# Performance work log

Hardware: AMD Instinct MI355X
Metric: run time of the kernel (lower is better)

Reference implementation:

```python
import jax, jax.numpy as jnp
import numpy as np

SCALE_FACTOR = 1.0
VIS_MAX = 1024


def setup_inputs() -> dict:
    key = jax.random.key(0)
    kq, kk, kv = jax.random.split(key, 3)
    B, C, H, W = 4, 256, 64, 64
    Q = jax.random.normal(kq, (B, C, H, W), dtype=jnp.float32)
    K = jax.random.normal(kk, (B, C, H, W), dtype=jnp.float32)
    V = jax.random.normal(kv, (B, C, H, W), dtype=jnp.float32)
    return {"Q": Q, "K": K, "V": V}


def reference(Q, K, V):
    # Q,K: [B,C,H,W] -> flatten spatial dims to HW
    B, C, H, W = Q.shape
    HW = H * W
    Q_flat = Q.reshape(B, C, HW).transpose(0, 2, 1)  # [B, HW, C]
    K_flat = K.reshape(B, C, HW)                      # [B, C, HW]
    # Full scaled score matrix [B, HW, HW]; argmax over keys reproduces the
    # chunked running-max/argmax (strict '>' update keeps first max, matching
    # jnp.argmax tie-breaking).
    S = jnp.einsum('bqc,bck->bqk', Q_flat, K_flat) * SCALE_FACTOR
    H_idx = jnp.argmax(S, axis=2).astype(jnp.int64)   # [B, HW]
    vis = min(VIS_MAX, HW)
    S_vis = S[:, :vis, :vis]                          # [B, vis, vis]
    return S_vis, H_idx
```

## Files before the change

### kernel.cpp

```cpp
#include <hip/hip_runtime.h>
#include <stdint.h>

#define B_   4
#define C_   256
#define HW_  4096
#define VIS_ 1024
#define KE_  768

using half8   = __attribute__((ext_vector_type(8))) _Float16;
using floatx4 = __attribute__((ext_vector_type(4))) float;

__device__ __forceinline__ unsigned mapf(float v) {
    unsigned u = __float_as_uint(v);
    return (u & 0x80000000u) ? ~u : (u | 0x80000000u);
}

__global__ void init_ws_kernel(unsigned long long* ws, int n) {
    int i = blockIdx.x * blockDim.x + threadIdx.x;
    if (i < n) ws[i] = 0ull;
}

__global__ void finalize_kernel(const unsigned long long* __restrict__ ws,
                                float* __restrict__ out1, int n) {
    int i = blockIdx.x * blockDim.x + threadIdx.x;
    if (i < n) {
        unsigned kinv = (unsigned)(ws[i] & 0xFFFFFFFFull);
        out1[i] = (float)(HW_ - 1 - (int)kinv);
    }
}


__global__ __launch_bounds__(256) void split_transpose_kernel(
    const float* __restrict__ Q, const float* __restrict__ K,
    _Float16* __restrict__ Aexp, _Float16* __restrict__ Bexp,
    unsigned long long* __restrict__ keys)
{
    __shared__ float tile[64][65];
    const int t = threadIdx.x;
    if (blockIdx.y == 0 && blockIdx.z == 0)
        keys[blockIdx.x * 256 + t] = 0ull;

    const int hw0 = blockIdx.x * 64;
    const int c0  = blockIdx.y * 64;
    const int z = blockIdx.z, b = z >> 1, which = z & 1;
    const float* src = (which ? K : Q) + (size_t)b * C_ * HW_;
    _Float16* dst = (which ? Bexp : Aexp) + (size_t)b * HW_ * KE_;

    #pragma unroll
    for (int i = 0; i < 4; ++i) {
        int c  = (t >> 4) + i * 16;
        int hw = (t & 15) * 4;
        float4 v = *(const float4*)(src + (size_t)(c0 + c) * HW_ + hw0 + hw);
        tile[c][hw] = v.x; tile[c][hw+1] = v.y; tile[c][hw+2] = v.z; tile[c][hw+3] = v.w;
    }
    __syncthreads();

    #pragma unroll
    for (int i = 0; i < 2; ++i) {
        int id  = t + i * 256;
        int row = id >> 3;
        int c8  = (id & 7) * 8;
        half8 h8, l8;
        #pragma unroll
        for (int j = 0; j < 8; ++j) {
            float v = tile[c8 + j][row];
            _Float16 h = (_Float16)v;
            h8[j] = h;
            l8[j] = (_Float16)(v - (float)h);
        }
        _Float16* base = dst + (size_t)(hw0 + row) * KE_ + c0 + c8;
        *(half8*)(base + 0 * C_) = h8;
        *(half8*)(base + 1 * C_) = which ? l8 : h8;
        *(half8*)(base + 2 * C_) = which ? h8 : l8;
    }
}

__device__ __forceinline__ void gl2lds16(const _Float16* g, _Float16* l) {
    __builtin_amdgcn_global_load_lds(
        (const __attribute__((address_space(1))) void*)g,
        (__attribute__((address_space(3))) void*)l, 16, 0, 0);
}


#define BARRIER __builtin_amdgcn_s_barrier()
#define LGKM0   asm volatile("s_waitcnt lgkmcnt(0)" ::: "memory")
#define VMC(n)  asm volatile("s_waitcnt vmcnt(" #n ")" ::: "memory")
#define SCHEDB  __builtin_amdgcn_sched_barrier(0)

__device__ __forceinline__ void stage_half(const _Float16* __restrict__ g,
                                           _Float16* lb, int t, int kbase)
{
    #pragma unroll
    for (int j = 0; j < 2; ++j) {
        const int c   = t + j * 512;
        const int row = c >> 2;
        const int ch  = (c & 3) ^ ((row >> 1) & 3);
        gl2lds16(g + (size_t)row * KE_ + kbase + ch * 8, lb + c * 8);
    }
}

template<int DB, int KH, int MQ>
__device__ __forceinline__ void ds_load_a(const _Float16* lds, int wave_m, int s,
                                          int quad, half8 (&a)[4]) {
    const _Float16* base = lds + (DB * 4 + KH) * 8192;
    #pragma unroll
    for (int mi = 0; mi < 4; ++mi) {
        int row = wave_m * 128 + MQ * 64 + mi * 16 + s;
        int ch  = quad ^ ((row >> 1) & 3);
        a[mi] = *(const half8*)(base + row * 32 + ch * 8);
    }
}

template<int DB, int KH>
__device__ __forceinline__ void ds_load_b(const _Float16* lds, int wave_n, int s,
                                          int quad, half8 (&bfr)[4]) {
    const _Float16* base = lds + (DB * 4 + 2 + KH) * 8192;
    #pragma unroll
    for (int ni = 0; ni < 4; ++ni) {
        int col = wave_n * 64 + ni * 16 + s;
        int ch  = quad ^ ((col >> 1) & 3);
        bfr[ni] = *(const half8*)(base + col * 32 + ch * 8);
    }
}

template<int MQ>
__device__ __forceinline__ void do_mfma(const half8 (&a)[4], const half8 (&bfr)[4],
                                        floatx4 (&acc)[8][4]) {
    __builtin_amdgcn_s_setprio(1);
    #pragma unroll
    for (int mi = 0; mi < 4; ++mi)
        #pragma unroll
        for (int ni = 0; ni < 4; ++ni)
            acc[MQ * 4 + mi][ni] = __builtin_amdgcn_mfma_f32_16x16x32_f16(
                a[mi], bfr[ni], acc[MQ * 4 + mi][ni], 0, 0, 0);
    __builtin_amdgcn_s_setprio(0);
}

__global__ __launch_bounds__(512, 1) void gemm_mfma_kernel(
    const _Float16* __restrict__ Aexp, const _Float16* __restrict__ Bexp,
    float* __restrict__ out0, unsigned long long* __restrict__ keys)
{
    __shared__ __align__(16) _Float16 lds[65536];

    const int t      = threadIdx.x;
    const int lane   = t & 63;
    const int wave   = t >> 6;
    const int quad   = lane >> 4;
    const int s      = lane & 15;
    const int wave_m = wave >> 2;
    const int wave_n = wave & 3;

    const int n    = blockIdx.x;
    const int wgid = (n & 7) * 128 + (n >> 3);
    const int kt   = wgid & 15;
    const int qt   = (wgid >> 4) & 15;
    const int b    = wgid >> 8;

    const _Float16* Agl = Aexp + (size_t)b * HW_ * KE_ + (size_t)(qt * 256) * KE_;
    const _Float16* Bgl = Bexp + (size_t)b * HW_ * KE_ + (size_t)(kt * 256) * KE_;

    stage_half(Agl, lds + 0 * 8192, t, 0);
    stage_half(Bgl, lds + 2 * 8192, t, 0);
    stage_half(Agl, lds + 1 * 8192, t, 32);
    stage_half(Bgl, lds + 3 * 8192, t, 32);
    stage_half(Agl, lds + 4 * 8192, t, 64);
    stage_half(Bgl, lds + 6 * 8192, t, 64);
    VMC(4);
    BARRIER; SCHEDB;

    half8 a[4], bfr[4];
    floatx4 acc[8][4] = {};

    #pragma unroll 1
    for (int it = 0; it < 5; ++it) {
        const int kb1 = (2 * it + 1) * 64;
        const int kb2 = kb1 + 64;
        const int kb3 = kb1 + 128;
        ds_load_a<0, 0, 0>(lds, wave_m, s, quad, a);
        ds_load_b<0, 0>(lds, wave_n, s, quad, bfr);
        stage_half(Agl, lds + 5 * 8192, t, kb1 + 32);
        BARRIER; LGKM0;
        do_mfma<0>(a, bfr, acc);
        BARRIER;
        ds_load_a<0, 0, 1>(lds, wave_m, s, quad, a);
        stage_half(Bgl, lds + 7 * 8192, t, kb1 + 32);
        BARRIER; LGKM0;
        do_mfma<1>(a, bfr, acc);
        BARRIER;
        ds_load_a<0, 1, 0>(lds, wave_m, s, quad, a);
        ds_load_b<0, 1>(lds, wave_n, s, quad, bfr);
        stage_half(Agl, lds + 0 * 8192, t, kb2);
        BARRIER; LGKM0;
        do_mfma<0>(a, bfr, acc);
        BARRIER;
        ds_load_a<0, 1, 1>(lds, wave_m, s, quad, a);
        stage_half(Bgl, lds + 2 * 8192, t, kb2);
        BARRIER; LGKM0;
        do_mfma<1>(a, bfr, acc);
        VMC(4);
        BARRIER; SCHEDB;
        ds_load_a<1, 0, 0>(lds, wave_m, s, quad, a);
        ds_load_b<1, 0>(lds, wave_n, s, quad, bfr);
        stage_half(Agl, lds + 1 * 8192, t, kb2 + 32);
        BARRIER; LGKM0;
        do_mfma<0>(a, bfr, acc);
        BARRIER;
        ds_load_a<1, 0, 1>(lds, wave_m, s, quad, a);
        stage_half(Bgl, lds + 3 * 8192, t, kb2 + 32);
        BARRIER; LGKM0;
        do_mfma<1>(a, bfr, acc);
        BARRIER;
        ds_load_a<1, 1, 0>(lds, wave_m, s, quad, a);
        ds_load_b<1, 1>(lds, wave_n, s, quad, bfr);
        stage_half(Agl, lds + 4 * 8192, t, kb3);
        BARRIER; LGKM0;
        do_mfma<0>(a, bfr, acc);
        BARRIER;
        ds_load_a<1, 1, 1>(lds, wave_m, s, quad, a);
        stage_half(Bgl, lds + 6 * 8192, t, kb3);
        BARRIER; LGKM0;
        do_mfma<1>(a, bfr, acc);
        VMC(4);
        BARRIER; SCHEDB;
    }

    stage_half(Agl, lds + 5 * 8192, t, 736);
    stage_half(Bgl, lds + 7 * 8192, t, 736);
    VMC(0);
    __syncthreads();

    ds_load_a<0, 0, 0>(lds, wave_m, s, quad, a);
    ds_load_b<0, 0>(lds, wave_n, s, quad, bfr);
    do_mfma<0>(a, bfr, acc);
    ds_load_a<0, 0, 1>(lds, wave_m, s, quad, a);
    do_mfma<1>(a, bfr, acc);
    ds_load_a<0, 1, 0>(lds, wave_m, s, quad, a);
    ds_load_b<0, 1>(lds, wave_n, s, quad, bfr);
    do_mfma<0>(a, bfr, acc);
    ds_load_a<0, 1, 1>(lds, wave_m, s, quad, a);
    do_mfma<1>(a, bfr, acc);
    ds_load_a<1, 0, 0>(lds, wave_m, s, quad, a);
    ds_load_b<1, 0>(lds, wave_n, s, quad, bfr);
    do_mfma<0>(a, bfr, acc);
    ds_load_a<1, 0, 1>(lds, wave_m, s, quad, a);
    do_mfma<1>(a, bfr, acc);
    ds_load_a<1, 1, 0>(lds, wave_m, s, quad, a);
    ds_load_b<1, 1>(lds, wave_n, s, quad, bfr);
    do_mfma<0>(a, bfr, acc);
    ds_load_a<1, 1, 1>(lds, wave_m, s, quad, a);
    do_mfma<1>(a, bfr, acc);

    if (qt < 4 && kt < 4) {
        #pragma unroll
        for (int mi8 = 0; mi8 < 8; ++mi8)
            #pragma unroll
            for (int r = 0; r < 4; ++r) {
                int grow = qt * 256 + wave_m * 128 + mi8 * 16 + quad * 4 + r;
                float* orow = out0 + ((size_t)b * VIS_ + grow) * VIS_ + kt * 256 + wave_n * 64;
                #pragma unroll
                for (int ni = 0; ni < 4; ++ni)
                    orow[ni * 16 + s] = acc[mi8][ni][r];
            }
    }

    __syncthreads();
    unsigned long long* red = (unsigned long long*)lds;

    #pragma unroll
    for (int mi8 = 0; mi8 < 8; ++mi8) {
        #pragma unroll
        for (int r = 0; r < 4; ++r) {
            float best = acc[mi8][0][r];
            int bcol = wave_n * 64 + s;
            #pragma unroll
            for (int ni = 1; ni < 4; ++ni) {
                float v = acc[mi8][ni][r];
                if (v > best) { best = v; bcol = wave_n * 64 + ni * 16 + s; }
            }
            int gcol = kt * 256 + bcol;
            unsigned long long key = ((unsigned long long)mapf(best) << 32)
                                   | (unsigned)(HW_ - 1 - gcol);
            #pragma unroll
            for (int m = 1; m < 16; m <<= 1) {
                unsigned long long o = __shfl_xor(key, m, 64);
                if (o > key) key = o;
            }
            if (s == 0)
                red[(wave_m * 128 + mi8 * 16 + quad * 4 + r) * 4 + wave_n] = key;
        }
    }
    __syncthreads();
    if (t < 256) {
        const unsigned long long* rr = red + t * 4;
        unsigned long long k0 = rr[0], k1 = rr[1], k2 = rr[2], k3 = rr[3];
        unsigned long long m01 = k0 > k1 ? k0 : k1;
        unsigned long long m23 = k2 > k3 ? k2 : k3;
        atomicMax(&keys[(size_t)b * HW_ + qt * 256 + t], m01 > m23 ? m01 : m23);
    }
}

#define BT   64
#define BK   32
#define LDP  68

__global__ __launch_bounds__(256) void gemm_argmax_kernel(
    const float* __restrict__ Q, const float* __restrict__ K,
    float* __restrict__ out0, unsigned long long* __restrict__ ws)
{
    __shared__ float As[BK][LDP];
    __shared__ float Bs[BK][LDP];
    __shared__ unsigned long long red[BT][17];

    const int t  = threadIdx.x;
    const int tx = t & 15;
    const int ty = t >> 4;
    const int k0 = blockIdx.x * BT;
    const int q0 = blockIdx.y * BT;
    const int b  = blockIdx.z;

    const float* Qb = Q + (size_t)b * C_ * HW_;
    const float* Kb = K + (size_t)b * C_ * HW_;

    float acc[4][4] = {{0.f},{0.f},{0.f},{0.f}};

    for (int c0 = 0; c0 < C_; c0 += BK) {
        #pragma unroll
        for (int i = 0; i < 2; ++i) {
            int idx = i * 256 + t;
            int row = idx >> 4;
            int col = (idx & 15) * 4;
            const float4 a  = *(const float4*)(Qb + (size_t)(c0 + row) * HW_ + q0 + col);
            const float4 bv = *(const float4*)(Kb + (size_t)(c0 + row) * HW_ + k0 + col);
            *(float4*)(&As[row][col]) = a;
            *(float4*)(&Bs[row][col]) = bv;
        }
        __syncthreads();
        #pragma unroll
        for (int cc = 0; cc < BK; ++cc) {
            const float4 av = *(const float4*)(&As[cc][ty * 4]);
            const float4 bv = *(const float4*)(&Bs[cc][tx * 4]);
            const float a_[4] = {av.x, av.y, av.z, av.w};
            const float b_[4] = {bv.x, bv.y, bv.z, bv.w};
            #pragma unroll
            for (int i = 0; i < 4; ++i)
                #pragma unroll
                for (int j = 0; j < 4; ++j)
                    acc[i][j] = fmaf(a_[i], b_[j], acc[i][j]);
        }
        __syncthreads();
    }

    if (q0 < VIS_ && k0 < VIS_) {
        #pragma unroll
        for (int i = 0; i < 4; ++i) {
            float4 v = make_float4(acc[i][0], acc[i][1], acc[i][2], acc[i][3]);
            size_t off = (size_t)b * VIS_ * VIS_ + (size_t)(q0 + ty * 4 + i) * VIS_ + (k0 + tx * 4);
            *(float4*)(out0 + off) = v;
        }
    }

    #pragma unroll
    for (int i = 0; i < 4; ++i) {
        float best = acc[i][0];
        int   bj   = 0;
        #pragma unroll
        for (int j = 1; j < 4; ++j)
            if (acc[i][j] > best) { best = acc[i][j]; bj = j; }
        int kidx = k0 + tx * 4 + bj;
        unsigned long long key = ((unsigned long long)mapf(best) << 32)
                               | (unsigned)(HW_ - 1 - kidx);
        red[ty * 4 + i][tx] = key;
    }
    __syncthreads();
    if (t < BT) {
        unsigned long long best = red[t][0];
        #pragma unroll
        for (int j = 1; j < 16; ++j) {
            unsigned long long v = red[t][j];
            if (v > best) best = v;
        }
        atomicMax(&ws[(size_t)b * HW_ + q0 + t], best);
    }
}

extern "C" void kernel_launch(void* const* d_in, const int* in_sizes, int n_in,
                              void* d_out, int out_size, void* d_ws, size_t ws_size,
                              hipStream_t stream) {
    const float* Q = (const float*)d_in[0];
    const float* K = (const float*)d_in[1];
    float* out0 = (float*)d_out;
    float* out1 = out0 + (size_t)B_ * VIS_ * VIS_;

    unsigned long long* keys = (unsigned long long*)d_ws;
    const size_t keys_bytes = (size_t)B_ * HW_ * 8;
    const size_t exp_elems  = (size_t)B_ * HW_ * KE_;
    const size_t need = keys_bytes + 2 * exp_elems * sizeof(_Float16);

    const int n = B_ * HW_;

    if (ws_size >= need) {
        _Float16* Aexp = (_Float16*)((char*)d_ws + keys_bytes);
        _Float16* Bexp = Aexp + exp_elems;
        split_transpose_kernel<<<dim3(HW_ / 64, C_ / 64, 2 * B_), 256, 0, stream>>>(Q, K, Aexp, Bexp, keys);
        gemm_mfma_kernel<<<dim3((HW_ / 256) * (HW_ / 256) * B_), 512, 0, stream>>>(Aexp, Bexp, out0, keys);
    } else {
        init_ws_kernel<<<(n + 255) / 256, 256, 0, stream>>>(keys, n);
        gemm_argmax_kernel<<<dim3(HW_ / BT, HW_ / BT, B_), 256, 0, stream>>>(Q, K, out0, keys);
    }

    finalize_kernel<<<(n + 255) / 256, 256, 0, stream>>>(keys, out1, n);
}
```

Before: 219.3 us.

## Restructure GEMM main loop into a 4-stage ring of 32-wide K slabs

Replaces the hand-unrolled double-buffered loop, which used paired 32-wide halves and 8 LDS slots, with a uniform 4-deep ring buffer. Each iteration consumes one K=32 slab (A and B) and prefetches the slab three steps ahead, with the vmcnt wait raised to keep more loads in flight. The aim is deeper global-to-LDS prefetch, more loads outstanding, and less code size. It also cuts out some intermediate barriers per K step. In exchange, the loop and its buffer-address computation become runtime-indexed, and there is one barrier pair per 32-wide slab.

```diff
diff --git a/kernel.cpp b/kernel.cpp
--- a/kernel.cpp
+++ b/kernel.cpp
@@ -99,10 +99,9 @@
     }
 }
 
-template<int DB, int KH, int MQ>
-__device__ __forceinline__ void ds_load_a(const _Float16* lds, int wave_m, int s,
+template<int MQ>
+__device__ __forceinline__ void ds_load_a(const _Float16* base, int wave_m, int s,
                                           int quad, half8 (&a)[4]) {
-    const _Float16* base = lds + (DB * 4 + KH) * 8192;
     #pragma unroll
     for (int mi = 0; mi < 4; ++mi) {
         int row = wave_m * 128 + MQ * 64 + mi * 16 + s;
@@ -111,10 +110,8 @@
     }
 }
 
-template<int DB, int KH>
-__device__ __forceinline__ void ds_load_b(const _Float16* lds, int wave_n, int s,
+__device__ __forceinline__ void ds_load_b(const _Float16* base, int wave_n, int s,
                                           int quad, half8 (&bfr)[4]) {
-    const _Float16* base = lds + (DB * 4 + 2 + KH) * 8192;
     #pragma unroll
     for (int ni = 0; ni < 4; ++ni) {
         int col = wave_n * 64 + ni * 16 + s;
@@ -160,95 +157,54 @@
     const _Float16* Bgl = Bexp + (size_t)b * HW_ * KE_ + (size_t)(kt * 256) * KE_;
 
     stage_half(Agl, lds + 0 * 8192, t, 0);
-    stage_half(Bgl, lds + 2 * 8192, t, 0);
-    stage_half(Agl, lds + 1 * 8192, t, 32);
+    stage_half(Bgl, lds + 1 * 8192, t, 0);
+    stage_half(Agl, lds + 2 * 8192, t, 32);
     stage_half(Bgl, lds + 3 * 8192, t, 32);
     stage_half(Agl, lds + 4 * 8192, t, 64);
-    stage_half(Bgl, lds + 6 * 8192, t, 64);
-    VMC(4);
+    stage_half(Bgl, lds + 5 * 8192, t, 64);
+    VMC(8);
     BARRIER; SCHEDB;
 
     half8 a[4], bfr[4];
     floatx4 acc[8][4] = {};
 
     #pragma unroll 1
-    for (int it = 0; it < 5; ++it) {
-        const int kb1 = (2 * it + 1) * 64;
-        const int kb2 = kb1 + 64;
-        const int kb3 = kb1 + 128;
-        ds_load_a<0, 0, 0>(lds, wave_m, s, quad, a);
-        ds_load_b<0, 0>(lds, wave_n, s, quad, bfr);
-        stage_half(Agl, lds + 5 * 8192, t, kb1 + 32);
+    for (int T = 0; T < 21; ++T) {
+        const int db  = T & 3;
+        const int db3 = (T + 3) & 3;
+        const _Float16* Ar = lds + (db * 2 + 0) * 8192;
+        const _Float16* Br = lds + (db * 2 + 1) * 8192;
+        _Float16* As = lds + (db3 * 2 + 0) * 8192;
+        _Float16* Bs = lds + (db3 * 2 + 1) * 8192;
+        const int kb3 = (T + 3) * 32;
+
+        ds_load_a<0>(Ar, wave_m, s, quad, a);
+        ds_load_b(Br, wave_n, s, quad, bfr);
+        stage_half(Agl, As, t, kb3);
         BARRIER; LGKM0;
         do_mfma<0>(a, bfr, acc);
         BARRIER;
-        ds_load_a<0, 0, 1>(lds, wave_m, s, quad, a);
-        stage_half(Bgl, lds + 7 * 8192, t, kb1 + 32);
+        ds_load_a<1>(Ar, wave_m, s, quad, a);
+        stage_half(Bgl, Bs, t, kb3);
         BARRIER; LGKM0;
         do_mfma<1>(a, bfr, acc);
-        BARRIER;
-        ds_load_a<0, 1, 0>(lds, wave_m, s, quad, a);
-        ds_load_b<0, 1>(lds, wave_n, s, quad, bfr);
-        stage_half(Agl, lds + 0 * 8192, t, kb2);
-        BARRIER; LGKM0;
+        VMC(8);
+        BARRIER; SCHEDB;
+    }
+
+    VMC(0);
+    __syncthreads();
+
+    #pragma unroll
+    for (int T = 21; T < 24; ++T) {
+        const _Float16* Ar = lds + ((T & 3) * 2 + 0) * 8192;
+        const _Float16* Br = lds + ((T & 3) * 2 + 1) * 8192;
+        ds_load_a<0>(Ar, wave_m, s, quad, a);
+        ds_load_b(Br, wave_n, s, quad, bfr);
         do_mfma<0>(a, bfr, acc);
-        BARRIER;
-        ds_load_a<0, 1, 1>(lds, wave_m, s, quad, a);
-        stage_half(Bgl, lds + 2 * 8192, t, kb2);
-        BARRIER; LGKM0;
+        ds_load_a<1>(Ar, wave_m, s, quad, a);
         do_mfma<1>(a, bfr, acc);
-        VMC(4);
-        BARRIER; SCHEDB;
-        ds_load_a<1, 0, 0>(lds, wave_m, s, quad, a);
-        ds_load_b<1, 0>(lds, wave_n, s, quad, bfr);
-        stage_half(Agl, lds + 1 * 8192, t, kb2 + 32);
-        BARRIER; LGKM0;
-        do_mfma<0>(a, bfr, acc);
-        BARRIER;
-        ds_load_a<1, 0, 1>(lds, wave_m, s, quad, a);
-        stage_half(Bgl, lds + 3 * 8192, t, kb2 + 32);
-        BARRIER; LGKM0;
-        do_mfma<1>(a, bfr, acc);
-        BARRIER;
-        ds_load_a<1, 1, 0>(lds, wave_m, s, quad, a);
-        ds_load_b<1, 1>(lds, wave_n, s, quad, bfr);
-        stage_half(Agl, lds + 4 * 8192, t, kb3);
-        BARRIER; LGKM0;
-        do_mfma<0>(a, bfr, acc);
-        BARRIER;
-        ds_load_a<1, 1, 1>(lds, wave_m, s, quad, a);
-        stage_half(Bgl, lds + 6 * 8192, t, kb3);
-        BARRIER; LGKM0;
-        do_mfma<1>(a, bfr, acc);
-        VMC(4);
-        BARRIER; SCHEDB;
-    }
-
-    stage_half(Agl, lds + 5 * 8192, t, 736);
-    stage_half(Bgl, lds + 7 * 8192, t, 736);
-    VMC(0);
-    __syncthreads();
-
-    ds_load_a<0, 0, 0>(lds, wave_m, s, quad, a);
-    ds_load_b<0, 0>(lds, wave_n, s, quad, bfr);
-    do_mfma<0>(a, bfr, acc);
-    ds_load_a<0, 0, 1>(lds, wave_m, s, quad, a);
-    do_mfma<1>(a, bfr, acc);
-    ds_load_a<0, 1, 0>(lds, wave_m, s, quad, a);
-    ds_load_b<0, 1>(lds, wave_n, s, quad, bfr);
-    do_mfma<0>(a, bfr, acc);
-    ds_load_a<0, 1, 1>(lds, wave_m, s, quad, a);
-    do_mfma<1>(a, bfr, acc);
-    ds_load_a<1, 0, 0>(lds, wave_m, s, quad, a);
-    ds_load_b<1, 0>(lds, wave_n, s, quad, bfr);
-    do_mfma<0>(a, bfr, acc);
-    ds_load_a<1, 0, 1>(lds, wave_m, s, quad, a);
-    do_mfma<1>(a, bfr, acc);
-    ds_load_a<1, 1, 0>(lds, wave_m, s, quad, a);
-    ds_load_b<1, 1>(lds, wave_n, s, quad, bfr);
-    do_mfma<0>(a, bfr, acc);
-    ds_load_a<1, 1, 1>(lds, wave_m, s, quad, a);
-    do_mfma<1>(a, bfr, acc);
+    }
 
     if (qt < 4 && kt < 4) {
         #pragma unroll
```

After: 214.9 us. 1.02x faster.
